# Kernel tuning notes

Hardware: AMD Instinct MI355X
Metric: run time of the kernel (lower is better)

## Reference

```python
import jax, jax.numpy as jnp
import numpy as np

NUM_HEAD = 16


def setup_inputs() -> dict:
    key = jax.random.key(0)
    ks = jax.random.split(key, 4)
    B, C, D = 2, 2048, 1024
    hidden_states = jax.random.normal(ks[0], (B, C, D), dtype=jnp.float32)
    attention_mask = jnp.zeros((B, 1, C, C), dtype=jnp.float32)
    Wqkv = jax.random.normal(ks[1], (D, 3 * D), dtype=jnp.float32) * (D ** -0.5)
    bqkv = jnp.zeros((3 * D,), dtype=jnp.float32)
    Wo = jax.random.normal(ks[2], (D, D), dtype=jnp.float32) * (D ** -0.5)
    bo = jnp.zeros((D,), dtype=jnp.float32)
    return {"hidden_states": hidden_states, "attention_mask": attention_mask,
            "Wqkv": Wqkv, "bqkv": bqkv, "Wo": Wo, "bo": bo}


def reference(hidden_states, attention_mask, Wqkv, bqkv, Wo, bo):
    B, C, D = hidden_states.shape
    H = NUM_HEAD
    hd = D // H
    scaling = hd ** -0.5

    qkv = hidden_states @ Wqkv + bqkv                      # [B, C, 3D]
    q, k, v = jnp.split(qkv, 3, axis=-1)
    # [B, C, H, hd] -> [B, H, C, hd]
    q = q.reshape(B, C, H, hd).transpose(0, 2, 1, 3)
    k = k.reshape(B, C, H, hd).transpose(0, 2, 1, 3)
    v = v.reshape(B, C, H, hd).transpose(0, 2, 1, 3)

    scores = jnp.einsum("bhqd,bhkd->bhqk", q, k) * scaling  # [B, H, C, C]
    causal = jnp.tril(jnp.ones((C, C), dtype=bool))[None, None]
    mask = jnp.where(causal, attention_mask, -jnp.inf)      # [B, 1, C, C]
    probs = jax.nn.softmax(scores + mask, axis=-1)
    out = jnp.einsum("bhqk,bhkd->bhqd", probs, v)           # [B, H, C, hd]
    out = out.transpose(0, 2, 1, 3).reshape(B, C, D)
    return out @ Wo + bo
```

## Files before the change

### kernel.cpp

```cpp
#include <hip/hip_runtime.h>
#include <hip/hip_bf16.h>
#include <cstdint>
#include <cstddef>

typedef __attribute__((ext_vector_type(8))) short short8;
typedef __attribute__((ext_vector_type(4))) float f32x4;
typedef __attribute__((ext_vector_type(16))) float f32x16;
typedef unsigned short u16;
typedef unsigned int u32;

#define B_ 2
#define C_ 2048
#define D_ 1024
#define H_ 16
#define HD_ 64

static __device__ __forceinline__ u16 f2b(float f) {
  u32 x = __builtin_bit_cast(u32, f);
  x += 0x7FFFu + ((x >> 16) & 1u);
  return (u16)(x >> 16);
}

__global__ void k_convert(const float* __restrict__ in, u16* __restrict__ out, int n) {
  int i = (blockIdx.x * blockDim.x + threadIdx.x) * 4;
  const int stride = gridDim.x * blockDim.x * 4;
  for (; i < n; i += stride) {
    float4 v = *reinterpret_cast<const float4*>(in + i);
    ushort4 o;
    o.x = f2b(v.x); o.y = f2b(v.y); o.z = f2b(v.z); o.w = f2b(v.w);
    *reinterpret_cast<ushort4*>(out + i) = o;
  }
}

__global__ void k_tconv(const float* __restrict__ in, u16* __restrict__ out, int R, int Cc) {
  __shared__ float tile[64][65];
  const int tC = blockIdx.x * 64;
  const int tR = blockIdx.y * 64;
  const int t = threadIdx.x;
  const int r0 = t >> 4;
  const int c0 = (t & 15) * 4;
#pragma unroll
  for (int ii = 0; ii < 4; ++ii) {
    int r = ii * 16 + r0;
    float4 v = *reinterpret_cast<const float4*>(&in[(size_t)(tR + r) * Cc + tC + c0]);
    tile[r][c0] = v.x; tile[r][c0 + 1] = v.y; tile[r][c0 + 2] = v.z; tile[r][c0 + 3] = v.w;
  }
  __syncthreads();
#pragma unroll
  for (int ii = 0; ii < 4; ++ii) {
    int c = ii * 16 + r0;
    ushort4 o;
    o.x = f2b(tile[c0 + 0][c]);
    o.y = f2b(tile[c0 + 1][c]);
    o.z = f2b(tile[c0 + 2][c]);
    o.w = f2b(tile[c0 + 3][c]);
    *reinterpret_cast<ushort4*>(&out[(size_t)(tC + c) * R + tR + c0]) = o;
  }
}

__global__ void k_maskflags(const float* __restrict__ mask, u32* __restrict__ flags) {
  const int bid = blockIdx.x;
  const int kt = bid & 31, qs = (bid >> 5) & 31, b = bid >> 10;
  const int t = threadIdx.x;
  const float* base = mask + ((size_t)b * C_ + qs * 64) * C_ + kt * 64;
  const int row = t >> 2, c0 = (t & 3) * 16;
  int any = 0;
#pragma unroll
  for (int i = 0; i < 4; ++i) {
    float4 v = *reinterpret_cast<const float4*>(base + (size_t)row * C_ + c0 + i * 4);
    any |= (v.x != 0.f) | (v.y != 0.f) | (v.z != 0.f) | (v.w != 0.f);
  }
  __shared__ int sh[4];
  const unsigned long long bal = __ballot(any);
  if ((t & 63) == 0) sh[t >> 6] = (bal != 0ull);
  __syncthreads();
  if (t == 0) flags[bid] = (u32)(sh[0] | sh[1] | sh[2] | sh[3]);
}

#define GLL16(gptr, lptr) __builtin_amdgcn_global_load_lds( \
    (const __attribute__((address_space(1))) u32*)(gptr),   \
    (__attribute__((address_space(3))) u32*)(lptr), 16, 0, 0)

template<int EPI, int BM>
__global__ __launch_bounds__(256) void k_gemm(
    const u16* __restrict__ A, const u16* __restrict__ Bt,
    int M, int N, int K, const float* __restrict__ bias,
    u16* __restrict__ Cq, u16* __restrict__ Ck, u16* __restrict__ Cv,
    float* __restrict__ Cf)
{
  constexpr int WCW = (BM == 128) ? 64 : 32;
  constexpr int NF = WCW / 16;
  __shared__ __align__(16) u16 As[BM * 64];
  __shared__ __align__(16) u16 Bs[128 * 64];
  const int t = threadIdx.x;
  const int l = t & 63, w = t >> 6;
  const int wr = (BM == 128) ? (w >> 1) : 0;
  const int wc = (BM == 128) ? (w & 1) : w;
  const int lr = l & 15, lg = l >> 4;
  const int swk = lr & 7;
  const int m0 = blockIdx.y * BM, n0 = blockIdx.x * 128;
  f32x4 acc[4][NF] = {};

  for (int k0 = 0; k0 < K; k0 += 64) {
#pragma unroll
    for (int s = 0; s < BM / 32; ++s) {
      const int u = s * 256 + t;
      const int row = u >> 3, slot = (u & 7) ^ (row & 7);
      GLL16(A + (size_t)(m0 + row) * K + k0 + (slot << 3), As + (u << 3));
    }
#pragma unroll
    for (int s = 0; s < 4; ++s) {
      const int u = s * 256 + t;
      const int row = u >> 3, slot = (u & 7) ^ (row & 7);
      GLL16(Bt + (size_t)(n0 + row) * K + k0 + (slot << 3), Bs + (u << 3));
    }
    __syncthreads();
    short8 af[2][4], bfr[2][NF];
#pragma unroll
    for (int s = 0; s < 2; ++s) {
#pragma unroll
      for (int m = 0; m < 4; ++m)
        af[s][m] = *reinterpret_cast<const short8*>(
            &As[((wr * 64 + m * 16 + lr) << 6) + (((s * 4 + lg) ^ swk) << 3)]);
#pragma unroll
      for (int n = 0; n < NF; ++n)
        bfr[s][n] = *reinterpret_cast<const short8*>(
            &Bs[((wc * WCW + n * 16 + lr) << 6) + (((s * 4 + lg) ^ swk) << 3)]);
    }
#pragma unroll
    for (int s = 0; s < 2; ++s)
#pragma unroll
      for (int m = 0; m < 4; ++m)
#pragma unroll
        for (int n = 0; n < NF; ++n)
          acc[m][n] = __builtin_amdgcn_mfma_f32_16x16x32_bf16(af[s][m], bfr[s][n], acc[m][n], 0, 0, 0);
    __syncthreads();
  }

#pragma unroll
  for (int m = 0; m < 4; ++m) {
    const int mg = m0 + wr * 64 + m * 16 + lg * 4;
    const int bq = mg >> 11, c0 = mg & 2047;
#pragma unroll
    for (int n = 0; n < NF; ++n) {
      const int ng = n0 + wc * WCW + n * 16 + lr;
      const float bia = bias[ng];
      if (EPI == 0) {
        const int reg = ng >> 10, d = ng & 1023, h = d >> 6, e = d & 63;
        if (reg == 2) {
          u16* vp = Cv + (((size_t)(bq * H_ + h) * HD_ + e) << 11) + c0;
#pragma unroll
          for (int j = 0; j < 4; ++j) vp[j] = f2b(acc[m][n][j] + bia);
        } else {
          u16* dst = (reg == 0) ? Cq : Ck;
#pragma unroll
          for (int j = 0; j < 4; ++j)
            dst[(((size_t)(bq * H_ + h) * C_ + c0 + j) << 6) + e] = f2b(acc[m][n][j] + bia);
        }
      } else {
#pragma unroll
        for (int j = 0; j < 4; ++j)
          Cf[(size_t)(mg + j) * N + ng] = acc[m][n][j] + bia;
      }
    }
  }
}

static __device__ __forceinline__ void stage_kv(
    const u16* __restrict__ Kbh, const u16* __restrict__ Vbh,
    u16* Kd, u16* Vd, int kt, int t)
{
#pragma unroll
  for (int ch = 0; ch < 2; ++ch) {
    const int u = ch * 256 + t;
    const int row = u >> 3, slot = (u & 7) ^ (row & 7);
    GLL16(Kbh + (((size_t)(kt * 64 + row)) << 6) + (slot << 3), Kd + (u << 3));
    GLL16(Vbh + (((size_t)row) << 11) + kt * 64 + (slot << 3), Vd + (u << 3));
  }
}

__global__ __launch_bounds__(256) void k_attn(
    const u16* __restrict__ Q, const u16* __restrict__ Kb, const u16* __restrict__ Vt,
    const float* __restrict__ mask, const u32* __restrict__ flags, u16* __restrict__ O)
{
  __shared__ __align__(16) u16 Kl[2][64 * 64];
  __shared__ __align__(16) u16 Vl[2][64 * 64];
  __shared__ __align__(16) u16 Sc[4][2304];
  const int bid = blockIdx.x;
  const int bh = bid & 31;
  const int qt = 15 - (bid >> 5);
  const int b = bh >> 4, h = bh & 15;
  const int t = threadIdx.x;
  const int l = t & 63, w = t >> 6;
  const int q = l & 31, hi = l >> 5;
  const int q7 = q & 7;

  const u16* Kbh = Kb + (size_t)bh * (C_ * HD_);
  const u16* Vbh = Vt + (size_t)bh * (HD_ * C_);
  char* Swb = reinterpret_cast<char*>(Sc[w]);

  const int ktb = 2 * qt + 2;
  const int q0w = qt * 128 + w * 32;
  const int qg = q0w + q;
  const int qmaxw = q0w + 31;

  short8 aq[4];
  {
    const u16* qp = Q + ((size_t)bh * C_ + qg) * HD_ + hi * 8;
#pragma unroll
    for (int kh = 0; kh < 4; ++kh) {
      short8 v = *reinterpret_cast<const short8*>(qp + kh * 16);
#pragma unroll
      for (int i = 0; i < 8; ++i) {
        const float f = __builtin_bit_cast(float, (u32)((u16)v[i]) << 16) * 0.125f;
        v[i] = (short)f2b(f);
      }
      aq[kh] = v;
    }
  }

  f32x16 oa0 = {}, oa1 = {};
  float mrun = -INFINITY, srun = 0.f;
  const float* mrow = mask + ((size_t)b * C_ + qg) * C_;
  const u32* fb = flags + (size_t)(b * 32 + (q0w >> 6)) * 32;

  stage_kv(Kbh, Vbh, Kl[0], Vl[0], 0, t);

#pragma unroll 1
  for (int kt = 0; kt < ktb; ++kt) {
    const int cur = kt & 1;
    __syncthreads();
    if (kt + 1 < ktb) stage_kv(Kbh, Vbh, Kl[cur ^ 1], Vl[cur ^ 1], kt + 1, t);
    if (kt * 64 > qmaxw) continue;

    const char* Kc = reinterpret_cast<const char*>(Kl[cur]);
    const char* Vc = reinterpret_cast<const char*>(Vl[cur]);

    f32x16 p0 = {}, p1 = {};
#pragma unroll
    for (int kh = 0; kh < 4; ++kh) {
      const int sl = ((2 * kh + hi) ^ q7) << 4;
      const short8 k0 = *reinterpret_cast<const short8*>(Kc + q * 128 + sl);
      const short8 k1 = *reinterpret_cast<const short8*>(Kc + (32 + q) * 128 + sl);
      p0 = __builtin_amdgcn_mfma_f32_32x32x16_bf16(k0, aq[kh], p0, 0, 0, 0);
      p1 = __builtin_amdgcn_mfma_f32_32x32x16_bf16(k1, aq[kh], p1, 0, 0, 0);
    }

    if (fb[kt]) {
      const float* mp = mrow + kt * 64 + 4 * hi;
#pragma unroll
      for (int g = 0; g < 4; ++g) {
        const float4 m0 = *reinterpret_cast<const float4*>(mp + 8 * g);
        const float4 m1 = *reinterpret_cast<const float4*>(mp + 32 + 8 * g);
        p0[4*g+0] += m0.x; p0[4*g+1] += m0.y; p0[4*g+2] += m0.z; p0[4*g+3] += m0.w;
        p1[4*g+0] += m1.x; p1[4*g+1] += m1.y; p1[4*g+2] += m1.z; p1[4*g+3] += m1.w;
      }
    }
    if (kt * 64 + 63 > q0w) {
#pragma unroll
      for (int r = 0; r < 16; ++r) {
        const int kl = kt * 64 + (r & 3) + 8 * (r >> 2) + 4 * hi;
        if (kl > qg) p0[r] = -INFINITY;
        if (kl + 32 > qg) p1[r] = -INFINITY;
      }
    }

    float pm = -INFINITY;
#pragma unroll
    for (int r = 0; r < 16; ++r) pm = fmaxf(pm, fmaxf(p0[r], p1[r]));
    pm = fmaxf(pm, __shfl_xor(pm, 32));
    const float mn = fmaxf(fmaxf(mrun, pm), -1e30f);
    const float rs = __expf(mrun - mn);
    float sum = 0.f;
#pragma unroll
    for (int r = 0; r < 16; ++r) {
      p0[r] = __expf(p0[r] - mn); sum += p0[r];
      p1[r] = __expf(p1[r] - mn); sum += p1[r];
    }
    sum += __shfl_xor(sum, 32);
    srun = srun * rs + sum;
    mrun = mn;
    oa0 *= rs; oa1 *= rs;

#pragma unroll
    for (int g = 0; g < 4; ++g) {
#pragma unroll
      for (int m = 0; m < 2; ++m) {
        u32 w0, w1;
        asm("v_cvt_pk_bf16_f32 %0, %1, %2" : "=v"(w0) : "v"(p0[4*g+2*m]), "v"(p0[4*g+2*m+1]));
        asm("v_cvt_pk_bf16_f32 %0, %1, %2" : "=v"(w1) : "v"(p1[4*g+2*m]), "v"(p1[4*g+2*m+1]));
        *reinterpret_cast<u32*>(Swb + q * 128 + ((g ^ q7) << 4) + 8 * hi + 4 * m) = w0;
        *reinterpret_cast<u32*>(Swb + q * 128 + (((4 + g) ^ q7) << 4) + 8 * hi + 4 * m) = w1;
      }
    }
    asm volatile("" ::: "memory");

#pragma unroll
    for (int ks = 0; ks < 4; ++ks) {
      const int sl = ((2 * ks + hi) ^ q7) << 4;
      const short8 bp = *reinterpret_cast<const short8*>(Swb + q * 128 + sl);
      const short8 v0 = *reinterpret_cast<const short8*>(Vc + q * 128 + sl);
      const short8 v1 = *reinterpret_cast<const short8*>(Vc + (32 + q) * 128 + sl);
      oa0 = __builtin_amdgcn_mfma_f32_32x32x16_bf16(v0, bp, oa0, 0, 0, 0);
      oa1 = __builtin_amdgcn_mfma_f32_32x32x16_bf16(v1, bp, oa1, 0, 0, 0);
    }
  }

  const float rinv = 1.f / srun;
#pragma unroll
  for (int g = 0; g < 4; ++g) {
    const int d0 = 8 * g + 4 * hi;
    const float a0 = oa0[4*g+0] * rinv, a1 = oa0[4*g+1] * rinv;
    const float a2 = oa0[4*g+2] * rinv, a3 = oa0[4*g+3] * rinv;
    const float b0 = oa1[4*g+0] * rinv, b1 = oa1[4*g+1] * rinv;
    const float b2 = oa1[4*g+2] * rinv, b3 = oa1[4*g+3] * rinv;
    u32 w0, w1, w2, w3;
    asm("v_cvt_pk_bf16_f32 %0, %1, %2" : "=v"(w0) : "v"(a0), "v"(a1));
    asm("v_cvt_pk_bf16_f32 %0, %1, %2" : "=v"(w1) : "v"(a2), "v"(a3));
    asm("v_cvt_pk_bf16_f32 %0, %1, %2" : "=v"(w2) : "v"(b0), "v"(b1));
    asm("v_cvt_pk_bf16_f32 %0, %1, %2" : "=v"(w3) : "v"(b2), "v"(b3));
    *reinterpret_cast<uint2*>(Swb + q * 144 + d0 * 2) = make_uint2(w0, w1);
    *reinterpret_cast<uint2*>(Swb + q * 144 + (d0 + 32) * 2) = make_uint2(w2, w3);
  }
  asm volatile("" ::: "memory");
  const int q2 = l >> 1, hf = l & 1;
  u16* orow = O + ((size_t)b * C_ + q0w + q2) * D_ + h * 64 + hf * 32;
#pragma unroll
  for (int i = 0; i < 4; ++i) {
    const short8 v = *reinterpret_cast<const short8*>(Swb + q2 * 144 + hf * 64 + i * 16);
    *reinterpret_cast<short8*>(orow + i * 8) = v;
  }
}

extern "C" void kernel_launch(void* const* d_in, const int* in_sizes, int n_in,
                              void* d_out, int out_size, void* d_ws, size_t ws_size,
                              hipStream_t stream) {
  const float* hs   = (const float*)d_in[0];
  const float* mask = (const float*)d_in[1];
  const float* Wqkv = (const float*)d_in[2];
  const float* bqkv = (const float*)d_in[3];
  const float* Wo   = (const float*)d_in[4];
  const float* bo   = (const float*)d_in[5];
  float* out = (float*)d_out;
  char* ws = (char*)d_ws;

  u16* hsb   = (u16*)(ws);
  u16* Wqkvt = (u16*)(ws + (8  << 20));
  u16* Wot   = (u16*)(ws + (14 << 20));
  u16* Qb    = (u16*)(ws + (16 << 20));
  u16* Kb    = (u16*)(ws + (24 << 20));
  u32* flags = (u32*)(ws + (32 << 20));
  u16* Vtb   = (u16*)(ws + (40 << 20));
  u16* AOb   = (u16*)(ws + (48 << 20));

  k_convert<<<2048, 256, 0, stream>>>(hs, hsb, 4096 * 1024);
  k_tconv<<<dim3(3072 / 64, 1024 / 64), 256, 0, stream>>>(Wqkv, Wqkvt, 1024, 3072);
  k_tconv<<<dim3(1024 / 64, 1024 / 64), 256, 0, stream>>>(Wo, Wot, 1024, 1024);
  k_maskflags<<<2048, 256, 0, stream>>>(mask, flags);
  k_gemm<0, 128><<<dim3(24, 32), 256, 0, stream>>>(hsb, Wqkvt, 4096, 3072, 1024, bqkv,
                                                   Qb, Kb, Vtb, nullptr);
  k_attn<<<512, 256, 0, stream>>>(Qb, Kb, Vtb, mask, flags, AOb);
  k_gemm<1, 64><<<dim3(8, 64), 256, 0, stream>>>(AOb, Wot, 4096, 1024, 1024, bo,
                                                 nullptr, nullptr, nullptr, out);
}
```

Baseline: 137.2 us.

## Split long causal attention query tiles across two KV segments with merge kernel

Query tiles 8-15, which have long causal KV ranges, are now split into two KV segments handled by separate blocks. The grid grows from 512 to 768 blocks to balance the causal workload. Each split block writes partial normalized bf16 outputs plus (max, sum) statistics, and a new merge kernel combines them with softmax rescaling. This cuts the tail latency of the longest blocks, at the cost of an extra launch, partial-buffer traffic, and some extra bf16 rounding. The workspace layout is reshuffled so the partial buffer reuses the hidden-state conversion area.

```diff
diff --git a/kernel.cpp b/kernel.cpp
--- a/kernel.cpp
+++ b/kernel.cpp
@@ -19,6 +19,9 @@
   u32 x = __builtin_bit_cast(u32, f);
   x += 0x7FFFu + ((x >> 16) & 1u);
   return (u16)(x >> 16);
+}
+static __device__ __forceinline__ float b2f(u16 v) {
+  return __builtin_bit_cast(float, (u32)v << 16);
 }
 
 __global__ void k_convert(const float* __restrict__ in, u16* __restrict__ out, int n) {
@@ -181,14 +184,23 @@
 
 __global__ __launch_bounds__(256) void k_attn(
     const u16* __restrict__ Q, const u16* __restrict__ Kb, const u16* __restrict__ Vt,
-    const float* __restrict__ mask, const u32* __restrict__ flags, u16* __restrict__ O)
+    const float* __restrict__ mask, const u32* __restrict__ flags,
+    u16* __restrict__ O, u16* __restrict__ Opart, float2* __restrict__ ml)
 {
   __shared__ __align__(16) u16 Kl[2][64 * 64];
   __shared__ __align__(16) u16 Vl[2][64 * 64];
   __shared__ __align__(16) u16 Sc[4][2304];
   const int bid = blockIdx.x;
   const int bh = bid & 31;
-  const int qt = 15 - (bid >> 5);
+  const int sidx = 23 - (bid >> 5);
+  int qt, seg, nseg;
+  if (sidx < 8) { qt = sidx; seg = 0; nseg = 1; }
+  else          { const int u = sidx - 8; qt = 8 + (u >> 1); seg = u & 1; nseg = 2; }
+  const int ntiles = 2 * qt + 2;
+  const int kt0 = seg * 16;
+  const int kt1 = seg ? ntiles : ((ntiles < 16) ? ntiles : 16);
+  const int slot = ((bh << 3) + (qt - 8)) * 2 + seg;
+
   const int b = bh >> 4, h = bh & 15;
   const int t = threadIdx.x;
   const int l = t & 63, w = t >> 6;
@@ -199,7 +211,6 @@
   const u16* Vbh = Vt + (size_t)bh * (HD_ * C_);
   char* Swb = reinterpret_cast<char*>(Sc[w]);
 
-  const int ktb = 2 * qt + 2;
   const int q0w = qt * 128 + w * 32;
   const int qg = q0w + q;
   const int qmaxw = q0w + 31;
@@ -212,7 +223,7 @@
       short8 v = *reinterpret_cast<const short8*>(qp + kh * 16);
 #pragma unroll
       for (int i = 0; i < 8; ++i) {
-        const float f = __builtin_bit_cast(float, (u32)((u16)v[i]) << 16) * 0.125f;
+        const float f = b2f((u16)v[i]) * 0.125f;
         v[i] = (short)f2b(f);
       }
       aq[kh] = v;
@@ -224,13 +235,13 @@
   const float* mrow = mask + ((size_t)b * C_ + qg) * C_;
   const u32* fb = flags + (size_t)(b * 32 + (q0w >> 6)) * 32;
 
-  stage_kv(Kbh, Vbh, Kl[0], Vl[0], 0, t);
+  stage_kv(Kbh, Vbh, Kl[0], Vl[0], kt0, t);
 
 #pragma unroll 1
-  for (int kt = 0; kt < ktb; ++kt) {
+  for (int kt = kt0; kt < kt1; ++kt) {
     const int cur = kt & 1;
     __syncthreads();
-    if (kt + 1 < ktb) stage_kv(Kbh, Vbh, Kl[cur ^ 1], Vl[cur ^ 1], kt + 1, t);
+    if (kt + 1 < kt1) stage_kv(Kbh, Vbh, Kl[cur ^ 1], Vl[cur ^ 1], kt + 1, t);
     if (kt * 64 > qmaxw) continue;
 
     const char* Kc = reinterpret_cast<const char*>(Kl[cur]);
@@ -324,11 +335,55 @@
   }
   asm volatile("" ::: "memory");
   const int q2 = l >> 1, hf = l & 1;
-  u16* orow = O + ((size_t)b * C_ + q0w + q2) * D_ + h * 64 + hf * 32;
+  if (nseg == 1) {
+    u16* orow = O + ((size_t)b * C_ + q0w + q2) * D_ + h * 64 + hf * 32;
+#pragma unroll
+    for (int i = 0; i < 4; ++i) {
+      const short8 v = *reinterpret_cast<const short8*>(Swb + q2 * 144 + hf * 64 + i * 16);
+      *reinterpret_cast<short8*>(orow + i * 8) = v;
+    }
+  } else {
+    u16* prow = Opart + (((size_t)slot * 128 + w * 32 + q2) << 6) + hf * 32;
+#pragma unroll
+    for (int i = 0; i < 4; ++i) {
+      const short8 v = *reinterpret_cast<const short8*>(Swb + q2 * 144 + hf * 64 + i * 16);
+      *reinterpret_cast<short8*>(prow + i * 8) = v;
+    }
+    if (hi == 0) ml[(size_t)slot * 128 + w * 32 + q] = make_float2(mrun, srun);
+  }
+}
+
+__global__ __launch_bounds__(256) void k_merge(
+    const u16* __restrict__ Opart, const float2* __restrict__ ml, u16* __restrict__ O)
+{
+  const int bid = blockIdx.x;
+  const int bh = bid & 31;
+  const int qt = 8 + (bid >> 5);
+  const int slot0 = ((bh << 3) + (qt - 8)) * 2;
+  const int b = bh >> 4, h = bh & 15;
+  const int t = threadIdx.x;
+  const int q = t >> 1, dh = t & 1;
+
+  const float2 v0 = ml[(size_t)slot0 * 128 + q];
+  const float2 v1 = ml[(size_t)(slot0 + 1) * 128 + q];
+  const float M = fmaxf(v0.x, v1.x);
+  const float a0 = __expf(v0.x - M) * v0.y;
+  const float a1 = __expf(v1.x - M) * v1.y;
+  const float rT = 1.f / (a0 + a1);
+  const float r0 = a0 * rT, r1 = a1 * rT;
+
+  const u16* p0 = Opart + (((size_t)slot0 * 128 + q) << 6) + dh * 32;
+  const u16* p1 = Opart + (((size_t)(slot0 + 1) * 128 + q) << 6) + dh * 32;
+  u16* orow = O + ((size_t)b * C_ + qt * 128 + q) * D_ + h * 64 + dh * 32;
 #pragma unroll
   for (int i = 0; i < 4; ++i) {
-    const short8 v = *reinterpret_cast<const short8*>(Swb + q2 * 144 + hf * 64 + i * 16);
-    *reinterpret_cast<short8*>(orow + i * 8) = v;
+    const short8 x0 = *reinterpret_cast<const short8*>(p0 + i * 8);
+    const short8 x1 = *reinterpret_cast<const short8*>(p1 + i * 8);
+    short8 y;
+#pragma unroll
+    for (int j = 0; j < 8; ++j)
+      y[j] = (short)f2b(r0 * b2f((u16)x0[j]) + r1 * b2f((u16)x1[j]));
+    *reinterpret_cast<short8*>(orow + i * 8) = y;
   }
 }
 
@@ -344,14 +399,16 @@
   float* out = (float*)d_out;
   char* ws = (char*)d_ws;
 
-  u16* hsb   = (u16*)(ws);
-  u16* Wqkvt = (u16*)(ws + (8  << 20));
-  u16* Wot   = (u16*)(ws + (14 << 20));
-  u16* Qb    = (u16*)(ws + (16 << 20));
-  u16* Kb    = (u16*)(ws + (24 << 20));
-  u32* flags = (u32*)(ws + (32 << 20));
-  u16* Vtb   = (u16*)(ws + (40 << 20));
-  u16* AOb   = (u16*)(ws + (48 << 20));
+  u16*    hsb   = (u16*)(ws);
+  u16*    Opart = (u16*)(ws);
+  u16*    Wqkvt = (u16*)(ws + (8  << 20));
+  float2* mlbuf = (float2*)(ws + (19 << 20));
+  u32*    flags = (u32*)(ws + (20 << 20) + (1 << 19));
+  u16*    Wot   = (u16*)(ws + (21 << 20));
+  u16*    Qb    = (u16*)(ws + (24 << 20));
+  u16*    Kb    = (u16*)(ws + (32 << 20));
+  u16*    Vtb   = (u16*)(ws + (40 << 20));
+  u16*    AOb   = (u16*)(ws + (48 << 20));
 
   k_convert<<<2048, 256, 0, stream>>>(hs, hsb, 4096 * 1024);
   k_tconv<<<dim3(3072 / 64, 1024 / 64), 256, 0, stream>>>(Wqkv, Wqkvt, 1024, 3072);
@@ -359,7 +416,8 @@
   k_maskflags<<<2048, 256, 0, stream>>>(mask, flags);
   k_gemm<0, 128><<<dim3(24, 32), 256, 0, stream>>>(hsb, Wqkvt, 4096, 3072, 1024, bqkv,
                                                    Qb, Kb, Vtb, nullptr);
-  k_attn<<<512, 256, 0, stream>>>(Qb, Kb, Vtb, mask, flags, AOb);
+  k_attn<<<768, 256, 0, stream>>>(Qb, Kb, Vtb, mask, flags, AOb, Opart, mlbuf);
+  k_merge<<<256, 256, 0, stream>>>(Opart, mlbuf, AOb);
   k_gemm<1, 64><<<dim3(8, 64), 256, 0, stream>>>(AOb, Wot, 4096, 1024, 1024, bo,
                                                  nullptr, nullptr, nullptr, out);
 }
```

Result: faster. 127.8 us (-6.8%).
